# Kernel optimization log

Hardware: AMD Instinct MI355X
Metric: run time of the kernel (lower is better)

Reference implementation:

```python
import jax, jax.numpy as jnp
import numpy as np
import math

B, D_MODEL, H, D_K, L = 24, 128, 8, 16, 512


def setup_inputs() -> dict:
    key = jax.random.key(0)
    ks = jax.random.split(key, 5)
    x = jax.random.normal(ks[0], (B, D_MODEL, L), dtype=jnp.float32)
    Wq = jax.random.normal(ks[1], (H, B, D_K, D_MODEL), dtype=jnp.float32)
    Wk = jax.random.normal(ks[2], (H, B, D_K, D_MODEL), dtype=jnp.float32)
    Wv = jax.random.normal(ks[3], (H, B, D_K, D_MODEL), dtype=jnp.float32)
    Wo = jax.random.normal(ks[4], (B, H * D_K, D_MODEL), dtype=jnp.float32)
    return {"x": x, "Wq": Wq, "Wk": Wk, "Wv": Wv, "Wo": Wo}


def reference(x, Wq, Wk, Wv, Wo):
    # Per-head, per-batch projections: [h,b,k,d] @ [b,d,l] -> [h,b,k,l]
    Q = jnp.einsum('hbkd,bdl->hbkl', Wq, x)
    K = jnp.einsum('hbkd,bdl->hbkl', Wk, x)
    V = jnp.einsum('hbkd,bdl->hbkl', Wv, x)
    # scores[h,b,l,m] = Q[:, :, :, l] . K[:, :, :, m]; torch softmax dim=1 of
    # the [B, L, L] score -> softmax over the QUERY axis l (axis=2 here).
    scores = jnp.einsum('hbkl,hbkm->hblm', Q, K) / math.sqrt(D_K)
    attn = jax.nn.softmax(scores, axis=2)
    # head_i = V @ attn : [h,b,v,l] @ [h,b,l,m] -> [h,b,v,m]
    heads = jnp.einsum('hbvl,hblm->hbvm', V, attn)
    # concat heads along channel dim: [b, h*v, L]
    head = heads.transpose(1, 0, 2, 3).reshape(B, H * D_K, L)
    # out = Wo @ head : [b, h*v, d_model] treated as [b,128,128] @ [b,128,L]
    out = jnp.einsum('bod,bdl->bol', Wo, head)
    return out
```

## Files before the change

kernel.cpp:

```cpp
#include <hip/hip_runtime.h>
#include <math.h>

#define NB 24
#define DM 128
#define NH 8
#define DK 16
#define LL 512
#define HB (NH * NB)

#define XTH_OFF 0
#define XTL_OFF 3145728
#define WHI_OFF 6291456
#define WLO_OFF 8650752
#define HT_OFF  11010048

typedef __attribute__((ext_vector_type(8))) short bf16x8;
typedef __attribute__((ext_vector_type(4))) float f32x4;
typedef __attribute__((ext_vector_type(4))) int   i32x4;

#define MFMA  __builtin_amdgcn_mfma_f32_16x16x32_bf16
#define EXP2  __builtin_amdgcn_exp2f
#define BPERM __builtin_amdgcn_ds_bpermute

static __device__ __forceinline__ unsigned bfr(float x) {
    return (__float_as_uint(x) + 0x8000u) & 0xffff0000u;
}

static __device__ __forceinline__ unsigned cvtpk(float a, float b) {
    unsigned r;
    asm("v_cvt_pk_bf16_f32 %0, %1, %2" : "=v"(r) : "v"(a), "v"(b));
    return r;
}

__global__ __launch_bounds__(256)
void prep(const float* __restrict__ x,
          const float* __restrict__ Wq,
          const float* __restrict__ Wk,
          const float* __restrict__ Wv,
          unsigned short* __restrict__ xthi,
          unsigned short* __restrict__ xtlo,
          unsigned short* __restrict__ whi,
          unsigned short* __restrict__ wlo)
{
    __shared__ float T[64][65];
    const int bid = blockIdx.x, tid = threadIdx.x;

    if (bid < 192) {
        const int b = bid >> 3, lc = bid & 7;
        #pragma unroll
        for (int half = 0; half < 2; ++half) {
            const int d0 = half << 6;
            const float* __restrict__ xb =
                x + (size_t)b * 65536 + (size_t)d0 * LL + lc * 64;
            if (half) __syncthreads();
            #pragma unroll
            for (int i = 0; i < 16; ++i) {
                const int idx = i * 256 + tid;
                T[idx >> 6][idx & 63] = xb[(size_t)(idx >> 6) * LL + (idx & 63)];
            }
            __syncthreads();
            #pragma unroll
            for (int i = 0; i < 8; ++i) {
                const int idx = (i * 256 + tid) * 2;
                const int l = idx >> 6, dd = idx & 63;
                const float v0 = T[dd][l], v1 = T[dd + 1][l];
                const unsigned h0 = bfr(v0), h1 = bfr(v1);
                const unsigned e0 = bfr(v0 - __uint_as_float(h0));
                const unsigned e1 = bfr(v1 - __uint_as_float(h1));
                const size_t o = (size_t)b * 65536 +
                                 (size_t)(lc * 64 + l) * DM + d0 + dd;
                *(unsigned*)(xthi + o) = (h0 >> 16) | (h1 & 0xffff0000u);
                *(unsigned*)(xtlo + o) = (e0 >> 16) | (e1 & 0xffff0000u);
            }
        }
    } else {
        const int w = bid - 192, hb = w / 3, mat = w - hb * 3;
        const float* __restrict__ src =
            (mat == 0 ? Wq : (mat == 1 ? Wk : Wv)) + (size_t)hb * 2048;
        unsigned short* __restrict__ dh = whi + (size_t)w * 2048;
        unsigned short* __restrict__ dl = wlo + (size_t)w * 2048;
        for (int i = tid; i < 1024; i += 256) {
            const float v0 = src[2 * i], v1 = src[2 * i + 1];
            const unsigned h0 = bfr(v0), h1 = bfr(v1);
            const unsigned e0 = bfr(v0 - __uint_as_float(h0));
            const unsigned e1 = bfr(v1 - __uint_as_float(h1));
            *(unsigned*)(dh + 2 * i) = (h0 >> 16) | (h1 & 0xffff0000u);
            *(unsigned*)(dl + 2 * i) = (e0 >> 16) | (e1 & 0xffff0000u);
        }
    }
}

static __device__ __forceinline__ void soft_pv(
    const f32x4& s0, const f32x4& s1, float tm, float& bar, float& sm,
    f32x4& O, const bf16x8& aV, int aLo, int aHi, bool up)
{
    const float nb = fmaxf(bar, tm + 32.f);
    const float f  = EXP2(bar - nb);
    bar = nb;
    const float e0 = EXP2(s0[0] - nb), e1 = EXP2(s0[1] - nb);
    const float e2 = EXP2(s0[2] - nb), e3 = EXP2(s0[3] - nb);
    const float e4 = EXP2(s1[0] - nb), e5 = EXP2(s1[1] - nb);
    const float e6 = EXP2(s1[2] - nb), e7 = EXP2(s1[3] - nb);
    const float sacc = ((e0 + e1) + (e2 + e3)) + ((e4 + e5) + (e6 + e7));
    sm = fmaf(sm, f, sacc);
    O *= f;
    const unsigned c0 = cvtpk(e0, e1), c1 = cvtpk(e2, e3);
    const unsigned c2 = cvtpk(e4, e5), c3 = cvtpk(e6, e7);
    const int p00 = BPERM(aLo, (int)c0), p02 = BPERM(aLo, (int)c2);
    const int p10 = BPERM(aLo, (int)c1), p12 = BPERM(aLo, (int)c3);
    const int p20 = BPERM(aHi, (int)c0), p22 = BPERM(aHi, (int)c2);
    const int p30 = BPERM(aHi, (int)c1), p32 = BPERM(aHi, (int)c3);
    i32x4 bi = { up ? p00 : p02, up ? p10 : p12,
                 up ? p20 : p22, up ? p30 : p32 };
    O = MFMA(aV, __builtin_bit_cast(bf16x8, bi), O, 0, 0, 0);
}

#define QK_STRIDE 40
#define V_STRIDE  520

__global__ __launch_bounds__(512)
void qkv_attn(const unsigned short* __restrict__ xthi,
              const unsigned short* __restrict__ xtlo,
              const unsigned short* __restrict__ whi,
              const unsigned short* __restrict__ wlo,
              unsigned short* __restrict__ ht)
{
    __shared__ unsigned short qs[LL * QK_STRIDE];
    __shared__ unsigned short ks[LL * QK_STRIDE];
    __shared__ unsigned short vs[DK * V_STRIDE];

    const int hb   = blockIdx.x;
    const int b    = hb % NB;
    const int wv   = threadIdx.x >> 6;
    const int lane = threadIdx.x & 63;
    const int g    = lane >> 4;
    const int mR   = lane & 15;
    const int l0   = wv * 64;

    {
        const unsigned short* __restrict__ wAh =
            whi + (size_t)hb * 6144 + mR * 128 + g * 8;
        const unsigned short* __restrict__ wAl =
            wlo + (size_t)hb * 6144 + mR * 128 + g * 8;
        const unsigned short* __restrict__ xh = xthi + (size_t)b * 65536 + g * 8;
        const unsigned short* __restrict__ xl = xtlo + (size_t)b * 65536 + g * 8;

        f32x4 C[3][4];
        #pragma unroll
        for (int m = 0; m < 3; ++m)
            #pragma unroll
            for (int t = 0; t < 4; ++t) C[m][t] = (f32x4){0.f, 0.f, 0.f, 0.f};

        #pragma unroll
        for (int kk = 0; kk < 4; ++kk) {
            bf16x8 bH[4], bL[4];
            #pragma unroll
            for (int t = 0; t < 4; ++t) {
                const size_t lo_ = (size_t)(l0 + t * 16 + mR) * DM + kk * 32;
                bH[t] = *(const bf16x8*)(xh + lo_);
                bL[t] = *(const bf16x8*)(xl + lo_);
            }
            #pragma unroll
            for (int m = 0; m < 3; ++m) {
                const bf16x8 aH = *(const bf16x8*)(wAh + m * 2048 + kk * 32);
                const bf16x8 aL = *(const bf16x8*)(wAl + m * 2048 + kk * 32);
                #pragma unroll
                for (int t = 0; t < 4; ++t) {
                    C[m][t] = MFMA(aH, bH[t], C[m][t], 0, 0, 0);
                    C[m][t] = MFMA(aH, bL[t], C[m][t], 0, 0, 0);
                    C[m][t] = MFMA(aL, bH[t], C[m][t], 0, 0, 0);
                }
            }
        }

        #pragma unroll
        for (int t = 0; t < 4; ++t) {
            const int l = l0 + t * 16 + mR;
            #pragma unroll
            for (int i = 0; i < 4; ++i)
                vs[(4 * g + i) * V_STRIDE + l] =
                    (unsigned short)(bfr(C[2][t][i]) >> 16);
        }
        #pragma unroll
        for (int m = 0; m < 2; ++m) {
            const float scale = m ? (0.25f * 1.44269504f) : 1.0f;
            unsigned short* __restrict__ dst = m ? ks : qs;
            #pragma unroll
            for (int t = 0; t < 4; ++t) {
                const int l = l0 + t * 16 + mR;
                ushort4 hi4, lo4;
                #pragma unroll
                for (int i = 0; i < 4; ++i) {
                    const float v = C[m][t][i] * scale;
                    const unsigned h = bfr(v);
                    const unsigned lw = bfr(v - __uint_as_float(h));
                    ((unsigned short*)&hi4)[i] = (unsigned short)(h >> 16);
                    ((unsigned short*)&lo4)[i] = (unsigned short)(lw >> 16);
                }
                *(ushort4*)(dst + l * QK_STRIDE + 4 * g)      = hi4;
                *(ushort4*)(dst + l * QK_STRIDE + 16 + 4 * g) = lo4;
            }
        }
    }

    __syncthreads();

    bf16x8 K0[2], K0s[2], K1[2], K1s[2];
    #pragma unroll
    for (int sub = 0; sub < 2; ++sub) {
        const unsigned short* Kr0 = ks + (wv * 64 + sub * 32 + mR) * QK_STRIDE;
        const unsigned short* Kr1 = Kr0 + 16 * QK_STRIDE;
        K0[sub]  = *(const bf16x8*)(Kr0 + g * 8);
        K0s[sub] = *(const bf16x8*)(Kr0 + (g ^ 2) * 8);
        K1[sub]  = *(const bf16x8*)(Kr1 + g * 8);
        K1s[sub] = *(const bf16x8*)(Kr1 + (g ^ 2) * 8);
    }

    const unsigned short* qrow = qs + mR * QK_STRIDE + g * 8;
    const unsigned short* vrow = vs + mR * V_STRIDE + g * 8;

    f32x4 O[2][2];
    float bar[2][2], sm[2][2];
    #pragma unroll
    for (int sub = 0; sub < 2; ++sub)
        #pragma unroll
        for (int gr = 0; gr < 2; ++gr) {
            O[sub][gr]   = (f32x4){0.f, 0.f, 0.f, 0.f};
            bar[sub][gr] = -1e30f;
            sm[sub][gr]  = 0.f;
        }

    const int aLo = ((g & 1) * 32 + mR) * 4;
    const int aHi = aLo + 64;
    const bool up = (g < 2);

    for (int l = 0; l < LL; l += 32) {
        const bf16x8 aQ0 = *(const bf16x8*)(qrow + l * QK_STRIDE);
        const bf16x8 aQ1 = *(const bf16x8*)(qrow + (l + 16) * QK_STRIDE);
        const bf16x8 aV  = *(const bf16x8*)(vrow + l);

        #pragma unroll
        for (int sub = 0; sub < 2; ++sub) {
            const f32x4 z = {0.f,0.f,0.f,0.f};
            f32x4 sA0 = MFMA(aQ0, K0[sub], z, 0,0,0);
            sA0 = MFMA(aQ0, K0s[sub], sA0, 0,0,0);
            f32x4 sB0 = MFMA(aQ0, K1[sub], z, 0,0,0);
            sB0 = MFMA(aQ0, K1s[sub], sB0, 0,0,0);
            f32x4 sA1 = MFMA(aQ1, K0[sub], z, 0,0,0);
            sA1 = MFMA(aQ1, K0s[sub], sA1, 0,0,0);
            f32x4 sB1 = MFMA(aQ1, K1[sub], z, 0,0,0);
            sB1 = MFMA(aQ1, K1s[sub], sB1, 0,0,0);

            float tmA = fmaxf(fmaxf(fmaxf(sA0[0],sA0[1]), fmaxf(sA0[2],sA0[3])),
                              fmaxf(fmaxf(sA1[0],sA1[1]), fmaxf(sA1[2],sA1[3])));
            float tmB = fmaxf(fmaxf(fmaxf(sB0[0],sB0[1]), fmaxf(sB0[2],sB0[3])),
                              fmaxf(fmaxf(sB1[0],sB1[1]), fmaxf(sB1[2],sB1[3])));
            tmA = fmaxf(tmA, __shfl_xor(tmA, 16, 64));
            tmA = fmaxf(tmA, __shfl_xor(tmA, 32, 64));
            tmB = fmaxf(tmB, __shfl_xor(tmB, 16, 64));
            tmB = fmaxf(tmB, __shfl_xor(tmB, 32, 64));

            const bool pA = __any(tmA + 64.f > bar[sub][0]);
            const bool pB = __any(tmB + 64.f > bar[sub][1]);
            if (pA) soft_pv(sA0, sA1, tmA, bar[sub][0], sm[sub][0],
                            O[sub][0], aV, aLo, aHi, up);
            if (pB) soft_pv(sB0, sB1, tmB, bar[sub][1], sm[sub][1],
                            O[sub][1], aV, aLo, aHi, up);
        }
    }

    const int h = hb / NB, bb = hb % NB;
    #pragma unroll
    for (int sub = 0; sub < 2; ++sub) {
        float s0 = sm[sub][0], s1 = sm[sub][1];
        s0 += __shfl_xor(s0, 16, 64);  s0 += __shfl_xor(s0, 32, 64);
        s1 += __shfl_xor(s1, 16, 64);  s1 += __shfl_xor(s1, 32, 64);
        const float i0 = 1.f / s0, i1 = 1.f / s1;

        unsigned short* __restrict__ ho =
            ht + (size_t)bb * 65536 +
            (size_t)(wv * 64 + sub * 32 + mR) * DM + h * 16 + 4 * g;
        ushort4 p0, p1;
        #pragma unroll
        for (int i = 0; i < 4; ++i) {
            ((unsigned short*)&p0)[i] =
                (unsigned short)(bfr(O[sub][0][i] * i0) >> 16);
            ((unsigned short*)&p1)[i] =
                (unsigned short)(bfr(O[sub][1][i] * i1) >> 16);
        }
        *(ushort4*)ho             = p0;
        *(ushort4*)(ho + 16 * DM) = p1;
    }
}

__global__ __launch_bounds__(256)
void out_mfma(const float* __restrict__ Wo,
              const unsigned short* __restrict__ ht,
              float* __restrict__ out)
{
    const int blk  = blockIdx.x;
    const int b    = blk >> 5;
    const int mq   = (blk >> 4) & 1;
    const int nq   = blk & 15;
    const int wv   = threadIdx.x >> 6;
    const int lane = threadIdx.x & 63;
    const int g = lane >> 4, mR = lane & 15;
    const int m0 = (mq * 4 + wv) * 16;
    const int n0 = nq * 32;

    const float* __restrict__ A =
        Wo + (size_t)b * 16384 + (size_t)(m0 + mR) * DM + g * 8;
    const unsigned short* __restrict__ B = ht + (size_t)b * 65536 + g * 8;

    f32x4 C0 = {0.f,0.f,0.f,0.f}, C1 = {0.f,0.f,0.f,0.f};
    #pragma unroll
    for (int kk = 0; kk < 4; ++kk) {
        const float4 f0 = *(const float4*)(A + kk * 32);
        const float4 f1 = *(const float4*)(A + kk * 32 + 4);
        i32x4 w;
        w[0] = (int)cvtpk(f0.x, f0.y);
        w[1] = (int)cvtpk(f0.z, f0.w);
        w[2] = (int)cvtpk(f1.x, f1.y);
        w[3] = (int)cvtpk(f1.z, f1.w);
        const bf16x8 aW = __builtin_bit_cast(bf16x8, w);
        const bf16x8 b0 = *(const bf16x8*)(B + (size_t)(n0 + mR) * DM + kk * 32);
        const bf16x8 b1 = *(const bf16x8*)(B + (size_t)(n0 + 16 + mR) * DM + kk * 32);
        C0 = MFMA(aW, b0, C0, 0, 0, 0);
        C1 = MFMA(aW, b1, C1, 0, 0, 0);
    }

    float* __restrict__ ob = out + (size_t)b * 65536 + (size_t)(m0 + 4 * g) * LL;
    #pragma unroll
    for (int i = 0; i < 4; ++i) {
        ob[(size_t)i * LL + n0 + mR]      = C0[i];
        ob[(size_t)i * LL + n0 + 16 + mR] = C1[i];
    }
}

extern "C" void kernel_launch(void* const* d_in, const int* in_sizes, int n_in,
                              void* d_out, int out_size, void* d_ws, size_t ws_size,
                              hipStream_t stream) {
    const float* x  = (const float*)d_in[0];
    const float* Wq = (const float*)d_in[1];
    const float* Wk = (const float*)d_in[2];
    const float* Wv = (const float*)d_in[3];
    const float* Wo = (const float*)d_in[4];
    float* out = (float*)d_out;

    char* ws = (char*)d_ws;
    unsigned short* xthi = (unsigned short*)(ws + XTH_OFF);
    unsigned short* xtlo = (unsigned short*)(ws + XTL_OFF);
    unsigned short* whi  = (unsigned short*)(ws + WHI_OFF);
    unsigned short* wlo  = (unsigned short*)(ws + WLO_OFF);
    unsigned short* ht   = (unsigned short*)(ws + HT_OFF);

    prep     <<<768,     256, 0, stream>>>(x, Wq, Wk, Wv, xthi, xtlo, whi, wlo);
    qkv_attn <<<HB,      512, 0, stream>>>(xthi, xtlo, whi, wlo, ht);
    out_mfma <<<NB * 32, 256, 0, stream>>>(Wo, ht, out);
}
```

Before: 115.2 us.

## Split attention blocks over key halves and fuse weight bf16 split into kernel

Each (head,batch) attention block is split into two blocks that each handle half of the key/output columns, doubling the grid to 384 blocks. This gives better coverage of the GPU's compute units, at the cost of recomputing the full Q and V projection in both blocks. The weight hi/lo bf16 splitting moves out of the prep kernel into the attention kernel, which reads fp32 weights directly. That drops the intermediate weight buffers and shrinks the prep grid. LDS use for K is halved and launch bounds now request 4 waves-per-EU occupancy.

New measurement: 129.9 us. 1.13x slower.

```diff
diff --git a/kernel.cpp b/kernel.cpp
--- a/kernel.cpp
+++ b/kernel.cpp
@@ -10,9 +10,7 @@
 
 #define XTH_OFF 0
 #define XTL_OFF 3145728
-#define WHI_OFF 6291456
-#define WLO_OFF 8650752
-#define HT_OFF  11010048
+#define HT_OFF  6291456
 
 typedef __attribute__((ext_vector_type(8))) short bf16x8;
 typedef __attribute__((ext_vector_type(4))) float f32x4;
@@ -32,60 +30,57 @@
     return r;
 }
 
+static __device__ __forceinline__ void wsplit(const float* __restrict__ p,
+                                              bf16x8& aH, bf16x8& aL) {
+    const float4 f0 = *(const float4*)p;
+    const float4 f1 = *(const float4*)(p + 4);
+    const float f[8] = {f0.x, f0.y, f0.z, f0.w, f1.x, f1.y, f1.z, f1.w};
+    i32x4 h, l;
+    #pragma unroll
+    for (int q = 0; q < 4; ++q) {
+        const unsigned h0 = bfr(f[2 * q]), h1 = bfr(f[2 * q + 1]);
+        const unsigned e0 = bfr(f[2 * q]     - __uint_as_float(h0));
+        const unsigned e1 = bfr(f[2 * q + 1] - __uint_as_float(h1));
+        h[q] = (int)((h0 >> 16) | (h1 & 0xffff0000u));
+        l[q] = (int)((e0 >> 16) | (e1 & 0xffff0000u));
+    }
+    aH = __builtin_bit_cast(bf16x8, h);
+    aL = __builtin_bit_cast(bf16x8, l);
+}
+
 __global__ __launch_bounds__(256)
 void prep(const float* __restrict__ x,
-          const float* __restrict__ Wq,
-          const float* __restrict__ Wk,
-          const float* __restrict__ Wv,
           unsigned short* __restrict__ xthi,
-          unsigned short* __restrict__ xtlo,
-          unsigned short* __restrict__ whi,
-          unsigned short* __restrict__ wlo)
+          unsigned short* __restrict__ xtlo)
 {
     __shared__ float T[64][65];
     const int bid = blockIdx.x, tid = threadIdx.x;
-
-    if (bid < 192) {
-        const int b = bid >> 3, lc = bid & 7;
-        #pragma unroll
-        for (int half = 0; half < 2; ++half) {
-            const int d0 = half << 6;
-            const float* __restrict__ xb =
-                x + (size_t)b * 65536 + (size_t)d0 * LL + lc * 64;
-            if (half) __syncthreads();
-            #pragma unroll
-            for (int i = 0; i < 16; ++i) {
-                const int idx = i * 256 + tid;
-                T[idx >> 6][idx & 63] = xb[(size_t)(idx >> 6) * LL + (idx & 63)];
-            }
-            __syncthreads();
-            #pragma unroll
-            for (int i = 0; i < 8; ++i) {
-                const int idx = (i * 256 + tid) * 2;
-                const int l = idx >> 6, dd = idx & 63;
-                const float v0 = T[dd][l], v1 = T[dd + 1][l];
-                const unsigned h0 = bfr(v0), h1 = bfr(v1);
-                const unsigned e0 = bfr(v0 - __uint_as_float(h0));
-                const unsigned e1 = bfr(v1 - __uint_as_float(h1));
-                const size_t o = (size_t)b * 65536 +
-                                 (size_t)(lc * 64 + l) * DM + d0 + dd;
-                *(unsigned*)(xthi + o) = (h0 >> 16) | (h1 & 0xffff0000u);
-                *(unsigned*)(xtlo + o) = (e0 >> 16) | (e1 & 0xffff0000u);
-            }
-        }
-    } else {
-        const int w = bid - 192, hb = w / 3, mat = w - hb * 3;
-        const float* __restrict__ src =
-            (mat == 0 ? Wq : (mat == 1 ? Wk : Wv)) + (size_t)hb * 2048;
-        unsigned short* __restrict__ dh = whi + (size_t)w * 2048;
-        unsigned short* __restrict__ dl = wlo + (size_t)w * 2048;
-        for (int i = tid; i < 1024; i += 256) {
-            const float v0 = src[2 * i], v1 = src[2 * i + 1];
+    const int b = bid >> 3, lc = bid & 7;
+
+    #pragma unroll
+    for (int half = 0; half < 2; ++half) {
+        const int d0 = half << 6;
+        const float* __restrict__ xb =
+            x + (size_t)b * 65536 + (size_t)d0 * LL + lc * 64;
+        if (half) __syncthreads();
+        #pragma unroll
+        for (int i = 0; i < 16; ++i) {
+            const int idx = i * 256 + tid;
+            T[idx >> 6][idx & 63] = xb[(size_t)(idx >> 6) * LL + (idx & 63)];
+        }
+        __syncthreads();
+        #pragma unroll
+        for (int i = 0; i < 8; ++i) {
+            const int idx = (i * 256 + tid) * 2;
+            const int l = idx >> 6, dd = idx & 63;
+            const float v0 = T[dd][l], v1 = T[dd + 1][l];
             const unsigned h0 = bfr(v0), h1 = bfr(v1);
             const unsigned e0 = bfr(v0 - __uint_as_float(h0));
             const unsigned e1 = bfr(v1 - __uint_as_float(h1));
-            *(unsigned*)(dh + 2 * i) = (h0 >> 16) | (h1 & 0xffff0000u);
-            *(unsigned*)(dl + 2 * i) = (e0 >> 16) | (e1 & 0xffff0000u);
+            const size_t o = (size_t)b * 65536 +
+                             (size_t)(lc * 64 + l) * DM + d0 + dd;
+            *(unsigned*)(xthi + o) = (h0 >> 16) | (h1 & 0xffff0000u);
+            *(unsigned*)(xtlo + o) = (e0 >> 16) | (e1 & 0xffff0000u);
         }
     }
 }
@@ -117,118 +112,143 @@
 
 #define QK_STRIDE 40
 #define V_STRIDE  520
-
-__global__ __launch_bounds__(512)
+#define KROWS     256
+
+__global__ __launch_bounds__(512, 4)
 void qkv_attn(const unsigned short* __restrict__ xthi,
               const unsigned short* __restrict__ xtlo,
-              const unsigned short* __restrict__ whi,
-              const unsigned short* __restrict__ wlo,
+              const float* __restrict__ Wq,
+              const float* __restrict__ Wk,
+              const float* __restrict__ Wv,
               unsigned short* __restrict__ ht)
 {
     __shared__ unsigned short qs[LL * QK_STRIDE];
-    __shared__ unsigned short ks[LL * QK_STRIDE];
+    __shared__ unsigned short ks[KROWS * QK_STRIDE];
     __shared__ unsigned short vs[DK * V_STRIDE];
 
-    const int hb   = blockIdx.x;
-    const int b    = hb % NB;
-    const int wv   = threadIdx.x >> 6;
-    const int lane = threadIdx.x & 63;
-    const int g    = lane >> 4;
-    const int mR   = lane & 15;
-    const int l0   = wv * 64;
+    const int hb    = blockIdx.x >> 1;
+    const int mhalf = blockIdx.x & 1;
+    const int b     = hb % NB;
+    const int wv    = threadIdx.x >> 6;
+    const int lane  = threadIdx.x & 63;
+    const int g     = lane >> 4;
+    const int mR    = lane & 15;
+    const int lQ    = wv * 64;
+    const int kloc  = wv * 32;
 
     {
-        const unsigned short* __restrict__ wAh =
-            whi + (size_t)hb * 6144 + mR * 128 + g * 8;
-        const unsigned short* __restrict__ wAl =
-            wlo + (size_t)hb * 6144 + mR * 128 + g * 8;
+        const float* __restrict__ wqp = Wq + (size_t)hb * 2048 + mR * 128 + g * 8;
+        const float* __restrict__ wkp = Wk + (size_t)hb * 2048 + mR * 128 + g * 8;
+        const float* __restrict__ wvp = Wv + (size_t)hb * 2048 + mR * 128 + g * 8;
         const unsigned short* __restrict__ xh = xthi + (size_t)b * 65536 + g * 8;
         const unsigned short* __restrict__ xl = xtlo + (size_t)b * 65536 + g * 8;
 
-        f32x4 C[3][4];
-        #pragma unroll
-        for (int m = 0; m < 3; ++m)
-            #pragma unroll
-            for (int t = 0; t < 4; ++t) C[m][t] = (f32x4){0.f, 0.f, 0.f, 0.f};
+        f32x4 CQ[4], CV[4], CK[2];
+        #pragma unroll
+        for (int t = 0; t < 4; ++t) {
+            CQ[t] = (f32x4){0.f, 0.f, 0.f, 0.f};
+            CV[t] = (f32x4){0.f, 0.f, 0.f, 0.f};
+        }
+        CK[0] = (f32x4){0.f, 0.f, 0.f, 0.f};
+        CK[1] = (f32x4){0.f, 0.f, 0.f, 0.f};
 
         #pragma unroll
         for (int kk = 0; kk < 4; ++kk) {
+            bf16x8 aH, aL;
+            {
+                bf16x8 kH[2], kL[2];
+                #pragma unroll
+                for (int t = 0; t < 2; ++t) {
+                    const size_t ro =
+                        (size_t)(mhalf * 256 + kloc + t * 16 + mR) * DM + kk * 32;
+                    kH[t] = *(const bf16x8*)(xh + ro);
+                    kL[t] = *(const bf16x8*)(xl + ro);
+                }
+                wsplit(wkp + kk * 32, aH, aL);
+                #pragma unroll
+                for (int t = 0; t < 2; ++t) {
+                    CK[t] = MFMA(aH, kH[t], CK[t], 0, 0, 0);
+                    CK[t] = MFMA(aH, kL[t], CK[t], 0, 0, 0);
+                    CK[t] = MFMA(aL, kH[t], CK[t], 0, 0, 0);
+                }
+            }
             bf16x8 bH[4], bL[4];
             #pragma unroll
             for (int t = 0; t < 4; ++t) {
-                const size_t lo_ = (size_t)(l0 + t * 16 + mR) * DM + kk * 32;
-                bH[t] = *(const bf16x8*)(xh + lo_);
-                bL[t] = *(const bf16x8*)(xl + lo_);
-            }
-            #pragma unroll
-            for (int m = 0; m < 3; ++m) {
-                const bf16x8 aH = *(const bf16x8*)(wAh + m * 2048 + kk * 32);
-                const bf16x8 aL = *(const bf16x8*)(wAl + m * 2048 + kk * 32);
-                #pragma unroll
-                for (int t = 0; t < 4; ++t) {
-                    C[m][t] = MFMA(aH, bH[t], C[m][t], 0, 0, 0);
-                    C[m][t] = MFMA(aH, bL[t], C[m][t], 0, 0, 0);
-                    C[m][t] = MFMA(aL, bH[t], C[m][t], 0, 0, 0);
-                }
+                const size_t ro = (size_t)(lQ + t * 16 + mR) * DM + kk * 32;
+                bH[t] = *(const bf16x8*)(xh + ro);
+                bL[t] = *(const bf16x8*)(xl + ro);
+            }
+            wsplit(wqp + kk * 32, aH, aL);
+            #pragma unroll
+            for (int t = 0; t < 4; ++t) {
+                CQ[t] = MFMA(aH, bH[t], CQ[t], 0, 0, 0);
+                CQ[t] = MFMA(aH, bL[t], CQ[t], 0, 0, 0);
+                CQ[t] = MFMA(aL, bH[t], CQ[t], 0, 0, 0);
+            }
+            wsplit(wvp + kk * 32, aH, aL);
+            #pragma unroll
+            for (int t = 0; t < 4; ++t) {
+                CV[t] = MFMA(aH, bH[t], CV[t], 0, 0, 0);
+                CV[t] = MFMA(aH, bL[t], CV[t], 0, 0, 0);
+                CV[t] = MFMA(aL, bH[t], CV[t], 0, 0, 0);
             }
         }
 
         #pragma unroll
         for (int t = 0; t < 4; ++t) {
-            const int l = l0 + t * 16 + mR;
+            const int l = lQ + t * 16 + mR;
             #pragma unroll
             for (int i = 0; i < 4; ++i)
                 vs[(4 * g + i) * V_STRIDE + l] =
-                    (unsigned short)(bfr(C[2][t][i]) >> 16);
-        }
-        #pragma unroll
-        for (int m = 0; m < 2; ++m) {
-            const float scale = m ? (0.25f * 1.44269504f) : 1.0f;
-            unsigned short* __restrict__ dst = m ? ks : qs;
-            #pragma unroll
-            for (int t = 0; t < 4; ++t) {
-                const int l = l0 + t * 16 + mR;
-                ushort4 hi4, lo4;
-                #pragma unroll
-                for (int i = 0; i < 4; ++i) {
-                    const float v = C[m][t][i] * scale;
-                    const unsigned h = bfr(v);
-                    const unsigned lw = bfr(v - __uint_as_float(h));
-                    ((unsigned short*)&hi4)[i] = (unsigned short)(h >> 16);
-                    ((unsigned short*)&lo4)[i] = (unsigned short)(lw >> 16);
-                }
-                *(ushort4*)(dst + l * QK_STRIDE + 4 * g)      = hi4;
-                *(ushort4*)(dst + l * QK_STRIDE + 16 + 4 * g) = lo4;
-            }
+                    (unsigned short)(bfr(CV[t][i]) >> 16);
+        }
+        #pragma unroll
+        for (int t = 0; t < 4; ++t) {
+            const int l = lQ + t * 16 + mR;
+            ushort4 hi4, lo4;
+            #pragma unroll
+            for (int i = 0; i < 4; ++i) {
+                const float v = CQ[t][i];
+                const unsigned h = bfr(v);
+                const unsigned lw = bfr(v - __uint_as_float(h));
+                ((unsigned short*)&hi4)[i] = (unsigned short)(h >> 16);
+                ((unsigned short*)&lo4)[i] = (unsigned short)(lw >> 16);
+            }
+            *(ushort4*)(qs + l * QK_STRIDE + 4 * g)      = hi4;
+            *(ushort4*)(qs + l * QK_STRIDE + 16 + 4 * g) = lo4;
+        }
+        #pragma unroll
+        for (int t = 0; t < 2; ++t) {
+            const int r = kloc + t * 16 + mR;
+            ushort4 hi4, lo4;
+            #pragma unroll
+            for (int i = 0; i < 4; ++i) {
+                const float v = CK[t][i] * (0.25f * 1.44269504f);
+                const unsigned h = bfr(v);
+                const unsigned lw = bfr(v - __uint_as_float(h));
+                ((unsigned short*)&hi4)[i] = (unsigned short)(h >> 16);
+                ((unsigned short*)&lo4)[i] = (unsigned short)(lw >> 16);
+            }
+            *(ushort4*)(ks + r * QK_STRIDE + 4 * g)      = hi4;
+            *(ushort4*)(ks + r * QK_STRIDE + 16 + 4 * g) = lo4;
         }
     }
 
     __syncthreads();
 
-    bf16x8 K0[2], K0s[2], K1[2], K1s[2];
-    #pragma unroll
-    for (int sub = 0; sub < 2; ++sub) {
-        const unsigned short* Kr0 = ks + (wv * 64 + sub * 32 + mR) * QK_STRIDE;
-        const unsigned short* Kr1 = Kr0 + 16 * QK_STRIDE;
-        K0[sub]  = *(const bf16x8*)(Kr0 + g * 8);
-        K0s[sub] = *(const bf16x8*)(Kr0 + (g ^ 2) * 8);
-        K1[sub]  = *(const bf16x8*)(Kr1 + g * 8);
-        K1s[sub] = *(const bf16x8*)(Kr1 + (g ^ 2) * 8);
-    }
+    const unsigned short* Kr0 = ks + (kloc + mR) * QK_STRIDE;
+    const unsigned short* Kr1 = Kr0 + 16 * QK_STRIDE;
+    const bf16x8 K0  = *(const bf16x8*)(Kr0 + g * 8);
+    const bf16x8 K0s = *(const bf16x8*)(Kr0 + (g ^ 2) * 8);
+    const bf16x8 K1  = *(const bf16x8*)(Kr1 + g * 8);
+    const bf16x8 K1s = *(const bf16x8*)(Kr1 + (g ^ 2) * 8);
 
     const unsigned short* qrow = qs + mR * QK_STRIDE + g * 8;
     const unsigned short* vrow = vs + mR * V_STRIDE + g * 8;
 
-    f32x4 O[2][2];
-    float bar[2][2], sm[2][2];
-    #pragma unroll
-    for (int sub = 0; sub < 2; ++sub)
-        #pragma unroll
-        for (int gr = 0; gr < 2; ++gr) {
-            O[sub][gr]   = (f32x4){0.f, 0.f, 0.f, 0.f};
-            bar[sub][gr] = -1e30f;
-            sm[sub][gr]  = 0.f;
-        }
+    f32x4 O0 = {0.f,0.f,0.f,0.f}, O1 = {0.f,0.f,0.f,0.f};
+    float bar0 = -1e30f, bar1 = -1e30f, sm0 = 0.f, sm1 = 0.f;
 
     const int aLo = ((g & 1) * 32 + mR) * 4;
     const int aHi = aLo + 64;
@@ -239,58 +259,43 @@
         const bf16x8 aQ1 = *(const bf16x8*)(qrow + (l + 16) * QK_STRIDE);
         const bf16x8 aV  = *(const bf16x8*)(vrow + l);
 
-        #pragma unroll
-        for (int sub = 0; sub < 2; ++sub) {
-            const f32x4 z = {0.f,0.f,0.f,0.f};
-            f32x4 sA0 = MFMA(aQ0, K0[sub], z, 0,0,0);
-            sA0 = MFMA(aQ0, K0s[sub], sA0, 0,0,0);
-            f32x4 sB0 = MFMA(aQ0, K1[sub], z, 0,0,0);
-            sB0 = MFMA(aQ0, K1s[sub], sB0, 0,0,0);
-            f32x4 sA1 = MFMA(aQ1, K0[sub], z, 0,0,0);
-            sA1 = MFMA(aQ1, K0s[sub], sA1, 0,0,0);
-            f32x4 sB1 = MFMA(aQ1, K1[sub], z, 0,0,0);
-            sB1 = MFMA(aQ1, K1s[sub], sB1, 0,0,0);
-
-            float tmA = fmaxf(fmaxf(fmaxf(sA0[0],sA0[1]), fmaxf(sA0[2],sA0[3])),
-                              fmaxf(fmaxf(sA1[0],sA1[1]), fmaxf(sA1[2],sA1[3])));
-            float tmB = fmaxf(fmaxf(fmaxf(sB0[0],sB0[1]), fmaxf(sB0[2],sB0[3])),
-                              fmaxf(fmaxf(sB1[0],sB1[1]), fmaxf(sB1[2],sB1[3])));
-            tmA = fmaxf(tmA, __shfl_xor(tmA, 16, 64));
-            tmA = fmaxf(tmA, __shfl_xor(tmA, 32, 64));
-            tmB = fmaxf(tmB, __shfl_xor(tmB, 16, 64));
-            tmB = fmaxf(tmB, __shfl_xor(tmB, 32, 64));
-
-            const bool pA = __any(tmA + 64.f > bar[sub][0]);
-            const bool pB = __any(tmB + 64.f > bar[sub][1]);
-            if (pA) soft_pv(sA0, sA1, tmA, bar[sub][0], sm[sub][0],
-                            O[sub][0], aV, aLo, aHi, up);
-            if (pB) soft_pv(sB0, sB1, tmB, bar[sub][1], sm[sub][1],
-                            O[sub][1], aV, aLo, aHi, up);
-        }
-    }
+        const f32x4 z = {0.f,0.f,0.f,0.f};
+        f32x4 sA0 = MFMA(aQ0, K0, z, 0,0,0);   sA0 = MFMA(aQ0, K0s, sA0, 0,0,0);
+        f32x4 sB0 = MFMA(aQ0, K1, z, 0,0,0);   sB0 = MFMA(aQ0, K1s, sB0, 0,0,0);
+        f32x4 sA1 = MFMA(aQ1, K0, z, 0,0,0);   sA1 = MFMA(aQ1, K0s, sA1, 0,0,0);
+        f32x4 sB1 = MFMA(aQ1, K1, z, 0,0,0);   sB1 = MFMA(aQ1, K1s, sB1, 0,0,0);
+
+        float tmA = fmaxf(fmaxf(fmaxf(sA0[0],sA0[1]), fmaxf(sA0[2],sA0[3])),
+                          fmaxf(fmaxf(sA1[0],sA1[1]), fmaxf(sA1[2],sA1[3])));
+        float tmB = fmaxf(fmaxf(fmaxf(sB0[0],sB0[1]), fmaxf(sB0[2],sB0[3])),
+                          fmaxf(fmaxf(sB1[0],sB1[1]), fmaxf(sB1[2],sB1[3])));
+        tmA = fmaxf(tmA, __shfl_xor(tmA, 16, 64));
+        tmA = fmaxf(tmA, __shfl_xor(tmA, 32, 64));
+        tmB = fmaxf(tmB, __shfl_xor(tmB, 16, 64));
+        tmB = fmaxf(tmB, __shfl_xor(tmB, 32, 64));
+
+        const bool pA = __any(tmA + 64.f > bar0);
+        const bool pB = __any(tmB + 64.f > bar1);
+        if (pA) soft_pv(sA0, sA1, tmA, bar0, sm0, O0, aV, aLo, aHi, up);
+        if (pB) soft_pv(sB0, sB1, tmB, bar1, sm1, O1, aV, aLo, aHi, up);
+    }
+
+    sm0 += __shfl_xor(sm0, 16, 64);  sm0 += __shfl_xor(sm0, 32, 64);
+    sm1 += __shfl_xor(sm1, 16, 64);  sm1 += __shfl_xor(sm1, 32, 64);
+    const float i0 = 1.f / sm0, i1 = 1.f / sm1;
 
     const int h = hb / NB, bb = hb % NB;
-    #pragma unroll
-    for (int sub = 0; sub < 2; ++sub) {
-        float s0 = sm[sub][0], s1 = sm[sub][1];
-        s0 += __shfl_xor(s0, 16, 64);  s0 += __shfl_xor(s0, 32, 64);
-        s1 += __shfl_xor(s1, 16, 64);  s1 += __shfl_xor(s1, 32, 64);
-        const float i0 = 1.f / s0, i1 = 1.f / s1;
-
-        unsigned short* __restrict__ ho =
-            ht + (size_t)bb * 65536 +
-            (size_t)(wv * 64 + sub * 32 + mR) * DM + h * 16 + 4 * g;
-        ushort4 p0, p1;
-        #pragma unroll
-        for (int i = 0; i < 4; ++i) {
-            ((unsigned short*)&p0)[i] =
-                (unsigned short)(bfr(O[sub][0][i] * i0) >> 16);
-            ((unsigned short*)&p1)[i] =
-                (unsigned short)(bfr(O[sub][1][i] * i1) >> 16);
-        }
-        *(ushort4*)ho             = p0;
-        *(ushort4*)(ho + 16 * DM) = p1;
-    }
+    const int mb = mhalf * 256 + kloc;
+    unsigned short* __restrict__ ho =
+        ht + (size_t)bb * 65536 + (size_t)(mb + mR) * DM + h * 16 + 4 * g;
+    ushort4 p0, p1;
+    #pragma unroll
+    for (int i = 0; i < 4; ++i) {
+        ((unsigned short*)&p0)[i] = (unsigned short)(bfr(O0[i] * i0) >> 16);
+        ((unsigned short*)&p1)[i] = (unsigned short)(bfr(O1[i] * i1) >> 16);
+    }
+    *(ushort4*)ho             = p0;
+    *(ushort4*)(ho + 16 * DM) = p1;
 }
 
 __global__ __launch_bounds__(256)
@@ -350,11 +355,9 @@
     char* ws = (char*)d_ws;
     unsigned short* xthi = (unsigned short*)(ws + XTH_OFF);
     unsigned short* xtlo = (unsigned short*)(ws + XTL_OFF);
-    unsigned short* whi  = (unsigned short*)(ws + WHI_OFF);
-    unsigned short* wlo  = (unsigned short*)(ws + WLO_OFF);
     unsigned short* ht   = (unsigned short*)(ws + HT_OFF);
 
-    prep     <<<768,     256, 0, stream>>>(x, Wq, Wk, Wv, xthi, xtlo, whi, wlo);
-    qkv_attn <<<HB,      512, 0, stream>>>(xthi, xtlo, whi, wlo, ht);
+    prep     <<<192,     256, 0, stream>>>(x, xthi, xtlo);
+    qkv_attn <<<HB * 2,  512, 0, stream>>>(xthi, xtlo, Wq, Wk, Wv, ht);
     out_mfma <<<NB * 32, 256, 0, stream>>>(Wo, ht, out);
 }
```
